# Kernel optimization log

Hardware: AMD Instinct MI355X
Metric: run time of the kernel (lower is better)

## Reference

```python
import jax, jax.numpy as jnp
import numpy as np

BN_EPS = 1e-5

def setup_inputs() -> dict:
    key = jax.random.key(0)
    k1, k2, k3, k4 = jax.random.split(key, 4)
    B, V, DI, DO = 4096, 64, 128, 128
    feat = jax.random.normal(k1, (B, V, DI), dtype=jnp.float32)
    adj = jax.random.uniform(k2, (V, V), dtype=jnp.float32)
    # per-vertex Linear weights (stacked): W[v] maps dim_in -> dim_out
    W = jax.random.normal(k3, (V, DI, DO), dtype=jnp.float32) * (1.0 / np.sqrt(DI))
    b = jax.random.normal(k4, (V, DO), dtype=jnp.float32) * 0.01
    gamma = jnp.ones((V, DO), dtype=jnp.float32)
    beta = jnp.zeros((V, DO), dtype=jnp.float32)
    return {"feat": feat, "adj": adj, "W": W, "b": b, "gamma": gamma, "beta": beta}

def reference(feat, adj, W, b, gamma, beta):
    # Per-vertex Linear as one grouped GEMM: [B,V,DI] x [V,DI,DO] -> [B,V,DO]
    h = jnp.einsum('bvi,vio->bvo', feat, W) + b[None, :, :]
    # BatchNorm1d (training mode): normalize over batch dim, per vertex & channel
    mu = jnp.mean(h, axis=0, keepdims=True)            # [1,V,DO]
    var = jnp.mean((h - mu) ** 2, axis=0, keepdims=True)  # biased variance
    h = (h - mu) * jax.lax.rsqrt(var + BN_EPS) * gamma[None] + beta[None]
    # adjacency mix: adj [V,V] applied to every batch element, then relu
    out = jnp.einsum('uv,bvo->buo', adj, h)
    return jax.nn.relu(out)
```

## Files before the change

kernel.cpp:

```cpp
#include <hip/hip_runtime.h>

#define BN 4096
#define VN 64
#define DI 128
#define DO 128

typedef __attribute__((ext_vector_type(8))) short short8;
typedef __attribute__((ext_vector_type(4))) float f32x4;

__device__ __forceinline__ float bf2f(unsigned short s) {
    return __uint_as_float(((unsigned)s) << 16);
}
__device__ __forceinline__ unsigned short f2bf(float f) {
    unsigned u = __float_as_uint(f);
    u += 0x7FFF + ((u >> 16) & 1);
    return (unsigned short)(u >> 16);
}
__device__ __forceinline__ unsigned pack_bf16_trunc(float lo, float hi) {
    return __builtin_amdgcn_perm(__float_as_uint(hi), __float_as_uint(lo), 0x07060302u);
}
__device__ __forceinline__ unsigned pack_bf16_rne(float lo, float hi) {
    return (unsigned)f2bf(lo) | ((unsigned)f2bf(hi) << 16);
}


__global__ __launch_bounds__(256) void k_prep(const float* __restrict__ W,
                                              const float* __restrict__ adj,
                                              unsigned short* __restrict__ Wt,
                                              unsigned short* __restrict__ adjbf) {
    const int t = threadIdx.x, blk = blockIdx.x;
    if (blk < 512) {
        const int v = blk >> 3, q = blk & 7;
        const float* Wv = W + (size_t)v * DI * DO;
        unsigned short* Wtv = Wt + (size_t)v * DI * DO;
        const int o = t & 127;
        const int i0 = q * 16 + (t >> 7) * 8;
        short8 s0;
#pragma unroll
        for (int j = 0; j < 8; ++j)
            s0[j] = (short)f2bf(Wv[(size_t)(i0 + j) * DO + o]);
        *(short8*)(Wtv + o * DI + i0) = s0;
    } else {
        short8 s0, s1;
#pragma unroll
        for (int j = 0; j < 8; ++j) s0[j] = (short)f2bf(adj[t * 16 + j]);
#pragma unroll
        for (int j = 0; j < 8; ++j) s1[j] = (short)f2bf(adj[t * 16 + 8 + j]);
        *(short8*)(adjbf + t * 16) = s0;
        *(short8*)(adjbf + t * 16 + 8) = s1;
    }
}

__global__ __launch_bounds__(256) void k_gemm1(const float* __restrict__ feat,
                                               const unsigned short* __restrict__ Wt,
                                               const float* __restrict__ bias,
                                               unsigned short* __restrict__ h,
                                               float* __restrict__ psA,
                                               float* __restrict__ psB) {
    __shared__ float ldsA[128 * 128];
    const int v = blockIdx.x;
    const int bt = blockIdx.y;
    const int tid = threadIdx.x;
    const int w = tid >> 6, lane = tid & 63;
    const int wm = w >> 1, wn = w & 1;
    const int quad = lane >> 4, l16 = lane & 15;

    const unsigned short* wbase = Wt + (size_t)v * (DI * DO)
                                + (size_t)(wn * 64 + l16) * DI + quad * 8;
    short8 bb[4][4];
#pragma unroll
    for (int ks = 0; ks < 4; ++ks)
#pragma unroll
        for (int nt = 0; nt < 4; ++nt)
            bb[ks][nt] = *(const short8*)(wbase + nt * (16 * DI) + ks * 32);

    {
        const int lrow = lane >> 5;
        const int lpos = lane & 31;
#pragma unroll
        for (int i = 0; i < 16; ++i) {
            const int row = w * 32 + 2 * i + lrow;
            const int gchunk = lpos ^ (row & 7);
            const float* src = feat + (size_t)(bt * 128 + row) * (VN * DI)
                             + v * DI + gchunk * 4;
            float* dst = &ldsA[(w * 32 + 2 * i) * 128];
            __builtin_amdgcn_global_load_lds(
                (const __attribute__((address_space(1))) void*)src,
                (__attribute__((address_space(3))) void*)dst, 16, 0, 0);
        }
    }
    __syncthreads();

    f32x4 acc[4][4];
#pragma unroll
    for (int rt = 0; rt < 4; ++rt)
#pragma unroll
        for (int nt = 0; nt < 4; ++nt) acc[rt][nt] = (f32x4){0.f, 0.f, 0.f, 0.f};

#pragma unroll
    for (int ks = 0; ks < 4; ++ks) {
        short8 aCur[4];
#pragma unroll
        for (int rt = 0; rt < 4; ++rt) {
            const int row = wm * 64 + rt * 16 + l16;
            const int xr = row & 7;
            const int c0 = ks * 8 + quad * 2;
            const f32x4 f0 = *(const f32x4*)&ldsA[row * 128 + ((c0    ) ^ xr) * 4];
            const f32x4 f1 = *(const f32x4*)&ldsA[row * 128 + ((c0 + 1) ^ xr) * 4];
            union { short8 s; unsigned u[4]; } pk;
            pk.u[0] = pack_bf16_trunc(f0[0], f0[1]);
            pk.u[1] = pack_bf16_trunc(f0[2], f0[3]);
            pk.u[2] = pack_bf16_trunc(f1[0], f1[1]);
            pk.u[3] = pack_bf16_trunc(f1[2], f1[3]);
            aCur[rt] = pk.s;
        }
#pragma unroll
        for (int rt = 0; rt < 4; ++rt)
#pragma unroll
            for (int nt = 0; nt < 4; ++nt)
                acc[rt][nt] = __builtin_amdgcn_mfma_f32_16x16x32_bf16(
                    aCur[rt], bb[ks][nt], acc[rt][nt], 0, 0, 0);
    }

    unsigned short* hblk = h + ((size_t)(bt * 64 + v) * 4 + w) * 4096;
#pragma unroll
    for (int nt = 0; nt < 4; ++nt) {
        const int col = wn * 64 + nt * 16 + l16;
        const float bv = bias[v * DO + col];
        float s = 0.f, sq = 0.f;
#pragma unroll
        for (int rt = 0; rt < 4; ++rt)
#pragma unroll
            for (int e = 0; e < 4; ++e) {
                float x = acc[rt][nt][e] + bv;
                acc[rt][nt][e] = x;
                s += x;
                sq += x * x;
            }
        s += __shfl_down(s, 32);  s += __shfl_down(s, 16);
        sq += __shfl_down(sq, 32); sq += __shfl_down(sq, 16);
        if (lane < 16) {
            const size_t pi = ((size_t)(v * 32 + bt) * 2 + wm) * 128 + col;
            psA[pi] = s;
            psB[pi] = sq;
        }
#pragma unroll
        for (int rt = 0; rt < 4; ++rt) {
            uint2 pk;
            pk.x = pack_bf16_rne(acc[rt][nt][0], acc[rt][nt][1]);
            pk.y = pack_bf16_rne(acc[rt][nt][2], acc[rt][nt][3]);
            *(uint2*)(hblk + (size_t)((nt * 4 + rt) * 64 + lane) * 4) = pk;
        }
    }
}

__global__ __launch_bounds__(128) void k_reduce(const float* __restrict__ psA,
                                                const float* __restrict__ psB,
                                                const float* __restrict__ gamma,
                                                const float* __restrict__ beta,
                                                float* __restrict__ scale,
                                                float* __restrict__ shift) {
    const int o = threadIdx.x;
    const int v = blockIdx.x;
    float s = 0.f, sq = 0.f;
#pragma unroll
    for (int p = 0; p < 64; ++p) {
        const size_t pi = ((size_t)v * 64 + p) * 128 + o;
        s += psA[pi];
        sq += psB[pi];
    }
    const float invB = 1.0f / (float)BN;
    const float mu = s * invB;
    const float var = sq * invB - mu * mu;
    const float sc = gamma[v * DO + o] * rsqrtf(var + 1e-5f);
    scale[v * DO + o] = sc;
    shift[v * DO + o] = beta[v * DO + o] - mu * sc;
}

__global__ __launch_bounds__(128) void k_c0(const float* __restrict__ adj,
                                            const float* __restrict__ shift,
                                            float* __restrict__ C0) {
    const int o = threadIdx.x;
    const int u = blockIdx.x;
    float c0 = 0.f;
#pragma unroll
    for (int v = 0; v < VN; ++v)
        c0 += adj[u * VN + v] * shift[v * DO + o];
    C0[u * DO + o] = c0;
}

__global__ __launch_bounds__(512, 4) void k_mix(const unsigned short* __restrict__ h,
                                                const float* __restrict__ scale,
                                                const unsigned short* __restrict__ adjbf,
                                                const float* __restrict__ C0,
                                                float* __restrict__ out) {
    __shared__ unsigned short hsT[4][DO][72];
    const int t = threadIdx.x;
    const int b0 = blockIdx.x * 4;
    const int bt = b0 >> 7;
    const int r = b0 & 127;
    const int swm = r >> 6, srt = (r >> 4) & 3, squad = (r >> 2) & 3;

#pragma unroll
    for (int c = 0; c < 16; ++c) {
        const int p = c * 512 + t;
        const int v = p >> 7, o = p & 127;
        const size_t off = (size_t)(bt * 64 + v) * 16384
                         + (size_t)(((swm * 2 + (o >> 6)) * 4 + ((o >> 4) & 3)) * 4 + srt) * 256
                         + (size_t)(squad * 16 + (o & 15)) * 4;
        const uint2 pk = *(const uint2*)(h + off);
        const float sc = scale[v * DO + o];
        hsT[0][o][v] = f2bf(bf2f((unsigned short)(pk.x & 0xFFFF)) * sc);
        hsT[1][o][v] = f2bf(bf2f((unsigned short)(pk.x >> 16)) * sc);
        hsT[2][o][v] = f2bf(bf2f((unsigned short)(pk.y & 0xFFFF)) * sc);
        hsT[3][o][v] = f2bf(bf2f((unsigned short)(pk.y >> 16)) * sc);
    }
    __syncthreads();

    const int w = t >> 6, lane = t & 63;
    const int bl = w >> 1, nh = w & 1;
    const int quad = lane >> 4, l16 = lane & 15;
    const int b = b0 + bl;

    short8 af[4][2];
#pragma unroll
    for (int mt = 0; mt < 4; ++mt)
#pragma unroll
        for (int ks = 0; ks < 2; ++ks)
            af[mt][ks] = *(const short8*)(adjbf + (mt * 16 + l16) * VN
                                          + ks * 32 + quad * 8);

    f32x4 acc[4][4];
#pragma unroll
    for (int mt = 0; mt < 4; ++mt)
#pragma unroll
        for (int nt = 0; nt < 4; ++nt) acc[mt][nt] = (f32x4){0.f, 0.f, 0.f, 0.f};

#pragma unroll
    for (int nt = 0; nt < 4; ++nt) {
        const unsigned short* bp = &hsT[bl][nh * 64 + nt * 16 + l16][quad * 8];
        short8 bf0 = *(const short8*)(bp);
        short8 bf1 = *(const short8*)(bp + 32);
#pragma unroll
        for (int mt = 0; mt < 4; ++mt) {
            acc[mt][nt] = __builtin_amdgcn_mfma_f32_16x16x32_bf16(
                af[mt][0], bf0, acc[mt][nt], 0, 0, 0);
            acc[mt][nt] = __builtin_amdgcn_mfma_f32_16x16x32_bf16(
                af[mt][1], bf1, acc[mt][nt], 0, 0, 0);
        }
    }

#pragma unroll
    for (int mt = 0; mt < 4; ++mt)
#pragma unroll
        for (int nt = 0; nt < 4; ++nt) {
            const int o = nh * 64 + nt * 16 + l16;
#pragma unroll
            for (int e = 0; e < 4; ++e) {
                const int u = mt * 16 + quad * 4 + e;
                out[((size_t)b * VN + u) * DO + o] =
                    fmaxf(acc[mt][nt][e] + C0[u * DO + o], 0.0f);
            }
        }
}

extern "C" void kernel_launch(void* const* d_in, const int* in_sizes, int n_in,
                              void* d_out, int out_size, void* d_ws, size_t ws_size,
                              hipStream_t stream) {
    const float* feat  = (const float*)d_in[0];
    const float* adj   = (const float*)d_in[1];
    const float* W     = (const float*)d_in[2];
    const float* bias  = (const float*)d_in[3];
    const float* gamma = (const float*)d_in[4];
    const float* beta  = (const float*)d_in[5];
    float* out = (float*)d_out;

    char* ws = (char*)d_ws;
    unsigned short* h     = (unsigned short*)ws;
    unsigned short* Wt    = (unsigned short*)(ws + 67108864ull);
    unsigned short* adjbf = (unsigned short*)(ws + 69206016ull);
    float* psA   = (float*)(ws + 69214208ull);
    float* psB   = psA + 524288;
    float* scale = psB + 524288;
    float* shift = scale + 8192;
    float* C0    = shift + 8192;

    k_prep<<<dim3(513), dim3(256), 0, stream>>>(W, adj, Wt, adjbf);
    k_gemm1<<<dim3(64, 32), dim3(256), 0, stream>>>(feat, Wt, bias, h, psA, psB);
    k_reduce<<<dim3(64), dim3(128), 0, stream>>>(psA, psB, gamma, beta, scale, shift);
    k_c0<<<dim3(64), dim3(128), 0, stream>>>(adj, shift, C0);
    k_mix<<<dim3(1024), dim3(512), 0, stream>>>(h, scale, adjbf, C0, out);
}
```

Baseline: 286.1 us.

## Retile grouped GEMM to 16-row by 8-vertex blocks with per-wave vertex pairs

```diff
diff --git a/kernel.cpp b/kernel.cpp
--- a/kernel.cpp
+++ b/kernel.cpp
@@ -57,99 +57,98 @@
                                                unsigned short* __restrict__ h,
                                                float* __restrict__ psA,
                                                float* __restrict__ psB) {
-    __shared__ float ldsA[128 * 128];
-    const int v = blockIdx.x;
-    const int bt = blockIdx.y;
+    __shared__ float ldsA[16 * 8 * 128];
+    const int vg = blockIdx.x;
+    const int rg = blockIdx.y;
     const int tid = threadIdx.x;
     const int w = tid >> 6, lane = tid & 63;
-    const int wm = w >> 1, wn = w & 1;
     const int quad = lane >> 4, l16 = lane & 15;
 
-    const unsigned short* wbase = Wt + (size_t)v * (DI * DO)
-                                + (size_t)(wn * 64 + l16) * DI + quad * 8;
-    short8 bb[4][4];
-#pragma unroll
-    for (int ks = 0; ks < 4; ++ks)
-#pragma unroll
-        for (int nt = 0; nt < 4; ++nt)
-            bb[ks][nt] = *(const short8*)(wbase + nt * (16 * DI) + ks * 32);
-
     {
-        const int lrow = lane >> 5;
-        const int lpos = lane & 31;
-#pragma unroll
-        for (int i = 0; i < 16; ++i) {
-            const int row = w * 32 + 2 * i + lrow;
-            const int gchunk = lpos ^ (row & 7);
-            const float* src = feat + (size_t)(bt * 128 + row) * (VN * DI)
-                             + v * DI + gchunk * 4;
-            float* dst = &ldsA[(w * 32 + 2 * i) * 128];
-            __builtin_amdgcn_global_load_lds(
-                (const __attribute__((address_space(1))) void*)src,
-                (__attribute__((address_space(3))) void*)dst, 16, 0, 0);
+        const int vi2 = lane >> 5;
+        const int cpos = lane & 31;
+#pragma unroll
+        for (int r = 0; r < 4; ++r) {
+            const int row = w * 4 + r;
+            const int gc = cpos ^ (row & 7);
+#pragma unroll
+            for (int q = 0; q < 4; ++q) {
+                const float* src = feat + (size_t)(rg * 16 + row) * (VN * DI)
+                                 + (vg * 8 + q * 2 + vi2) * DI + gc * 4;
+                float* dst = &ldsA[(row * 8 + q * 2) * 128];
+                __builtin_amdgcn_global_load_lds(
+                    (const __attribute__((address_space(1))) void*)src,
+                    (__attribute__((address_space(3))) void*)dst, 16, 0, 0);
+            }
         }
     }
     __syncthreads();
 
-    f32x4 acc[4][4];
-#pragma unroll
-    for (int rt = 0; rt < 4; ++rt)
-#pragma unroll
-        for (int nt = 0; nt < 4; ++nt) acc[rt][nt] = (f32x4){0.f, 0.f, 0.f, 0.f};
-
-#pragma unroll
-    for (int ks = 0; ks < 4; ++ks) {
-        short8 aCur[4];
-#pragma unroll
-        for (int rt = 0; rt < 4; ++rt) {
-            const int row = wm * 64 + rt * 16 + l16;
-            const int xr = row & 7;
+    const int bt = rg >> 3, wm = (rg >> 2) & 1, rt = rg & 3;
+
+#pragma unroll
+    for (int vv = 0; vv < 2; ++vv) {
+        const int vi = w * 2 + vv;
+        const int v = vg * 8 + vi;
+
+        short8 aF[4];
+#pragma unroll
+        for (int ks = 0; ks < 4; ++ks) {
+            const int xr = l16 & 7;
             const int c0 = ks * 8 + quad * 2;
-            const f32x4 f0 = *(const f32x4*)&ldsA[row * 128 + ((c0    ) ^ xr) * 4];
-            const f32x4 f1 = *(const f32x4*)&ldsA[row * 128 + ((c0 + 1) ^ xr) * 4];
+            const f32x4 f0 = *(const f32x4*)&ldsA[(l16 * 8 + vi) * 128 + ((c0    ) ^ xr) * 4];
+            const f32x4 f1 = *(const f32x4*)&ldsA[(l16 * 8 + vi) * 128 + ((c0 + 1) ^ xr) * 4];
             union { short8 s; unsigned u[4]; } pk;
             pk.u[0] = pack_bf16_trunc(f0[0], f0[1]);
             pk.u[1] = pack_bf16_trunc(f0[2], f0[3]);
             pk.u[2] = pack_bf16_trunc(f1[0], f1[1]);
             pk.u[3] = pack_bf16_trunc(f1[2], f1[3]);
-            aCur[rt] = pk.s;
-        }
-#pragma unroll
-        for (int rt = 0; rt < 4; ++rt)
-#pragma unroll
-            for (int nt = 0; nt < 4; ++nt)
-                acc[rt][nt] = __builtin_amdgcn_mfma_f32_16x16x32_bf16(
-                    aCur[rt], bb[ks][nt], acc[rt][nt], 0, 0, 0);
-    }
-
-    unsigned short* hblk = h + ((size_t)(bt * 64 + v) * 4 + w) * 4096;
-#pragma unroll
-    for (int nt = 0; nt < 4; ++nt) {
-        const int col = wn * 64 + nt * 16 + l16;
-        const float bv = bias[v * DO + col];
-        float s = 0.f, sq = 0.f;
-#pragma unroll
-        for (int rt = 0; rt < 4; ++rt)
+            aF[ks] = pk.s;
+        }
+
+        f32x4 acc[8];
+#pragma unroll
+        for (int j = 0; j < 8; ++j) acc[j] = (f32x4){0.f, 0.f, 0.f, 0.f};
+
+        const unsigned short* wb = Wt + (size_t)v * (DI * DO)
+                                 + (size_t)l16 * DI + quad * 8;
+#pragma unroll
+        for (int ks = 0; ks < 4; ++ks) {
+            short8 bb[8];
+#pragma unroll
+            for (int j = 0; j < 8; ++j)
+                bb[j] = *(const short8*)(wb + j * (16 * DI) + ks * 32);
+#pragma unroll
+            for (int j = 0; j < 8; ++j)
+                acc[j] = __builtin_amdgcn_mfma_f32_16x16x32_bf16(
+                    aF[ks], bb[j], acc[j], 0, 0, 0);
+        }
+
+        unsigned short* hbase = h + ((size_t)(bt * 64 + v) * 4 + wm * 2) * 4096;
+#pragma unroll
+        for (int j = 0; j < 8; ++j) {
+            const int col = j * 16 + l16;
+            const float bv = bias[v * DO + col];
+            float s = 0.f, sq = 0.f;
 #pragma unroll
             for (int e = 0; e < 4; ++e) {
-                float x = acc[rt][nt][e] + bv;
-                acc[rt][nt][e] = x;
+                float x = acc[j][e] + bv;
+                acc[j][e] = x;
                 s += x;
                 sq += x * x;
             }
-        s += __shfl_down(s, 32);  s += __shfl_down(s, 16);
-        sq += __shfl_down(sq, 32); sq += __shfl_down(sq, 16);
-        if (lane < 16) {
-            const size_t pi = ((size_t)(v * 32 + bt) * 2 + wm) * 128 + col;
-            psA[pi] = s;
-            psB[pi] = sq;
-        }
-#pragma unroll
-        for (int rt = 0; rt < 4; ++rt) {
+            s += __shfl_down(s, 32);  s += __shfl_down(s, 16);
+            sq += __shfl_down(sq, 32); sq += __shfl_down(sq, 16);
+            if (lane < 16) {
+                const size_t pi = ((size_t)v * 256 + rg) * 128 + col;
+                psA[pi] = s;
+                psB[pi] = sq;
+            }
             uint2 pk;
-            pk.x = pack_bf16_rne(acc[rt][nt][0], acc[rt][nt][1]);
-            pk.y = pack_bf16_rne(acc[rt][nt][2], acc[rt][nt][3]);
-            *(uint2*)(hblk + (size_t)((nt * 4 + rt) * 64 + lane) * 4) = pk;
+            pk.x = pack_bf16_rne(acc[j][0], acc[j][1]);
+            pk.y = pack_bf16_rne(acc[j][2], acc[j][3]);
+            *(uint2*)(hbase + (size_t)(j >> 2) * 4096
+                      + (size_t)(((j & 3) * 4 + rt) * 64 + lane) * 4) = pk;
         }
     }
 }
@@ -163,9 +162,9 @@
     const int o = threadIdx.x;
     const int v = blockIdx.x;
     float s = 0.f, sq = 0.f;
-#pragma unroll
-    for (int p = 0; p < 64; ++p) {
-        const size_t pi = ((size_t)v * 64 + p) * 128 + o;
+#pragma unroll 8
+    for (int p = 0; p < 256; ++p) {
+        const size_t pi = ((size_t)v * 256 + p) * 128 + o;
         s += psA[pi];
         sq += psB[pi];
     }
@@ -280,13 +279,13 @@
     unsigned short* Wt    = (unsigned short*)(ws + 67108864ull);
     unsigned short* adjbf = (unsigned short*)(ws + 69206016ull);
     float* psA   = (float*)(ws + 69214208ull);
-    float* psB   = psA + 524288;
-    float* scale = psB + 524288;
+    float* psB   = psA + 2097152;
+    float* scale = psB + 2097152;
     float* shift = scale + 8192;
     float* C0    = shift + 8192;
 
     k_prep<<<dim3(513), dim3(256), 0, stream>>>(W, adj, Wt, adjbf);
-    k_gemm1<<<dim3(64, 32), dim3(256), 0, stream>>>(feat, Wt, bias, h, psA, psB);
+    k_gemm1<<<dim3(8, 256), dim3(256), 0, stream>>>(feat, Wt, bias, h, psA, psB);
     k_reduce<<<dim3(64), dim3(128), 0, stream>>>(psA, psB, gamma, beta, scale, shift);
     k_c0<<<dim3(64), dim3(128), 0, stream>>>(adj, shift, C0);
     k_mix<<<dim3(1024), dim3(512), 0, stream>>>(h, scale, adjbf, C0, out);
```

Result: slower. 340.2 us (+18.9%).
